# Kernel optimization log

Measured on AMD Instinct MI355X. Metric: run time of the kernel, lower is better.

Reference implementation:

```python
import jax, jax.numpy as jnp
import numpy as np

N = 100000   # nodes
E = 1600000  # edges
D = 128      # d_model
H = 8        # heads
HD = D // H  # head dim
T = 8        # edge types


def setup_inputs() -> dict:
    key = jax.random.key(0)
    ks = jax.random.split(key, 16)
    s = 0.02
    inp = {
        "x": jax.random.normal(ks[0], (N, D), jnp.float32),
        "edge_index": jax.random.randint(ks[1], (2, E), 0, N, jnp.int32),
        "edge_type": jax.random.randint(ks[2], (E,), 0, T, jnp.int32),
        "Wq": jax.random.normal(ks[3], (D, D), jnp.float32) * s,
        "bq": jnp.zeros((D,), jnp.float32),
        "Wk": jax.random.normal(ks[4], (D, D), jnp.float32) * s,
        "bk": jnp.zeros((D,), jnp.float32),
        "Wv": jax.random.normal(ks[5], (D, D), jnp.float32) * s,
        "bv": jnp.zeros((D,), jnp.float32),
        "Wo": jax.random.normal(ks[6], (D, D), jnp.float32) * s,
        "bo": jnp.zeros((D,), jnp.float32),
        "edge_bias": jax.random.normal(ks[7], (T, H), jnp.float32) * s,
        "W1": jax.random.normal(ks[8], (D, D), jnp.float32) * s,
        "b1": jnp.zeros((D,), jnp.float32),
        "W2": jax.random.normal(ks[9], (D, D), jnp.float32) * s,
        "b2": jnp.zeros((D,), jnp.float32),
        "g1": jnp.ones((D,), jnp.float32),
        "be1": jnp.zeros((D,), jnp.float32),
        "g2": jnp.ones((D,), jnp.float32),
        "be2": jnp.zeros((D,), jnp.float32),
    }
    return inp


def _layernorm(x, g, b, eps=1e-5):
    m = jnp.mean(x, axis=-1, keepdims=True)
    v = jnp.mean((x - m) ** 2, axis=-1, keepdims=True)
    return (x - m) * jax.lax.rsqrt(v + eps) * g + b


def reference(x, edge_index, edge_type, Wq, bq, Wk, bk, Wv, bv, Wo, bo,
              edge_bias, W1, b1, W2, b2, g1, be1, g2, be2):
    n = x.shape[0]
    scale = HD ** -0.5
    Q = (x @ Wq + bq).reshape(n, H, HD)
    K = (x @ Wk + bk).reshape(n, H, HD)
    V = (x @ Wv + bv).reshape(n, H, HD)
    src, dst = edge_index[0], edge_index[1]
    # per-edge attention logits [E, H]
    attn = jnp.sum(Q[dst] * K[src], axis=-1) * scale + edge_bias[edge_type]
    # segment softmax grouped by destination node
    mx = jax.ops.segment_max(attn, dst, num_segments=n)  # [n, H]
    ex = jnp.exp(attn - mx[dst])
    sm = jax.ops.segment_sum(ex, dst, num_segments=n)
    a = ex / (sm[dst] + 1e-16)
    # weighted scatter-add of values
    out = jax.ops.segment_sum(a[..., None] * V[src], dst, num_segments=n)
    out = out.reshape(n, D) @ Wo + bo
    x = _layernorm(x + out, g1, be1)
    ffn = jax.nn.gelu(x @ W1 + b1, approximate=False) @ W2 + b2
    return _layernorm(x + ffn, g2, be2)
```

## Files before the change

### kernel.cpp

```cpp
#include <hip/hip_runtime.h>
#include <math.h>

#define D   128
#define NH  8
#define CAP 64

typedef __attribute__((ext_vector_type(8))) short  bfrag;
typedef __attribute__((ext_vector_type(4))) float  f32x4;

__device__ __forceinline__ unsigned short f2bf(float f) {
  unsigned int u = __float_as_uint(f);
  unsigned int r = u + 0x7fffu + ((u >> 16) & 1u);
  return (unsigned short)(r >> 16);
}
__device__ __forceinline__ float bf2f(unsigned short b) {
  return __uint_as_float(((unsigned int)b) << 16);
}

__device__ __forceinline__ int swz(int r, int kb) {
  return r * 256 + (kb ^ ((r & 7) << 4));
}

__global__ void prew_kernel(const float* __restrict__ W0, const float* __restrict__ W1,
                            const float* __restrict__ W2, const float* __restrict__ W3,
                            const float* __restrict__ W4, const float* __restrict__ W5,
                            unsigned short* __restrict__ img)
{
  const float* Wm[6] = {W0, W1, W2, W3, W4, W5};
  const float* W = Wm[blockIdx.x];
  unsigned short* ih = img + (size_t)blockIdx.x * 32768;
  unsigned short* il = ih + 16384;
  for (int s = threadIdx.x; s < 16384; s += 256) {
    int j = s & 7, l = (s >> 3) & 63, kk = (s >> 9) & 3, cbg = s >> 11;
    int c = cbg * 16 + (l & 15);
    int k = kk * 32 + (l >> 4) * 8 + j;
    float v = W[k * D + c];
    unsigned short h = f2bf(v);
    ih[s] = h;
    il[s] = f2bf(v - bf2f(h));
  }
}

__device__ __forceinline__ void stage_x(const float* __restrict__ A, char* lds,
                                        int r0, int n, int t)
{
#pragma unroll
  for (int i = 0; i < 8; ++i) {
    int f = i * 256 + t;
    int r = f >> 5;
    int c = (f & 31) * 4;
    float4 v = make_float4(0.f, 0.f, 0.f, 0.f);
    int row = r0 + r;
    if (row < n) v = *(const float4*)&A[(size_t)row * D + c];
    unsigned short h0 = f2bf(v.x), h1 = f2bf(v.y), h2 = f2bf(v.z), h3 = f2bf(v.w);
    ushort4 hv; hv.x = h0; hv.y = h1; hv.z = h2; hv.w = h3;
    ushort4 lv;
    lv.x = f2bf(v.x - bf2f(h0)); lv.y = f2bf(v.y - bf2f(h1));
    lv.z = f2bf(v.z - bf2f(h2)); lv.w = f2bf(v.w - bf2f(h3));
    int o = swz(r, c * 2);
    *(ushort4*)(lds + o)         = hv;
    *(ushort4*)(lds + 16384 + o) = lv;
  }
}

__device__ __forceinline__ void gemm_tile(const unsigned short* __restrict__ imgh,
                                          const unsigned short* __restrict__ imgl,
                                          const char* lds, f32x4 (&acc)[4][2],
                                          int wave, int lane)
{
  bfrag bh[2][4], bl[2][4];
#pragma unroll
  for (int cb = 0; cb < 2; ++cb)
#pragma unroll
    for (int kk = 0; kk < 4; ++kk) {
      int f = ((wave * 2 + cb) * 4 + kk) * 64 + lane;
      bh[cb][kk] = *(const bfrag*)&imgh[f * 8];
      bl[cb][kk] = *(const bfrag*)&imgl[f * 8];
    }
#pragma unroll
  for (int rb = 0; rb < 4; ++rb)
#pragma unroll
    for (int kk = 0; kk < 4; ++kk) {
      int o = swz(rb * 16 + (lane & 15), kk * 64 + (lane >> 4) * 16);
      bfrag ah = *(const bfrag*)(lds + o);
      bfrag al = *(const bfrag*)(lds + 16384 + o);
#pragma unroll
      for (int cb = 0; cb < 2; ++cb) {
        acc[rb][cb] = __builtin_amdgcn_mfma_f32_16x16x32_bf16(ah, bh[cb][kk], acc[rb][cb], 0, 0, 0);
        acc[rb][cb] = __builtin_amdgcn_mfma_f32_16x16x32_bf16(al, bh[cb][kk], acc[rb][cb], 0, 0, 0);
        acc[rb][cb] = __builtin_amdgcn_mfma_f32_16x16x32_bf16(ah, bl[cb][kk], acc[rb][cb], 0, 0, 0);
      }
    }
}

__device__ __forceinline__ void zero_acc(f32x4 (&acc)[4][2]) {
#pragma unroll
  for (int rb = 0; rb < 4; ++rb)
#pragma unroll
    for (int cb = 0; cb < 2; ++cb) {
      f32x4 z = {0.f, 0.f, 0.f, 0.f};
      acc[rb][cb] = z;
    }
}

__global__ __launch_bounds__(256, 2) void qkv_kernel(
    const float* __restrict__ x, const unsigned short* __restrict__ img,
    const float* __restrict__ bq, const float* __restrict__ bk, const float* __restrict__ bv,
    unsigned short* __restrict__ Q, unsigned short* __restrict__ K,
    unsigned short* __restrict__ V, int n)
{
  __shared__ char lds[49152];
  const int t = threadIdx.x, wave = t >> 6, lane = t & 63;
  const int r0 = blockIdx.x * 64;
  stage_x(x, lds, r0, n, t);
  __syncthreads();

  const float* bs[3] = {bq, bk, bv};
  unsigned short* Os[3] = {Q, K, V};
  unsigned short* scH = (unsigned short*)(lds + 32768);

  for (int m = 0; m < 3; ++m) {
    f32x4 acc[4][2];
    zero_acc(acc);
    gemm_tile(img + (size_t)m * 32768, img + (size_t)m * 32768 + 16384, lds, acc, wave, lane);
    float b0 = bs[m][wave * 32 + (lane & 15)];
    float b1 = bs[m][wave * 32 + 16 + (lane & 15)];
    __syncthreads();
#pragma unroll
    for (int rb = 0; rb < 4; ++rb)
#pragma unroll
      for (int cb = 0; cb < 2; ++cb) {
        float bb = cb ? b1 : b0;
        int col = wave * 32 + cb * 16 + (lane & 15);
#pragma unroll
        for (int r = 0; r < 4; ++r) {
          int row = rb * 16 + (lane >> 4) * 4 + r;
          scH[row * D + col] = f2bf(acc[rb][cb][r] + bb);
        }
      }
    __syncthreads();
#pragma unroll
    for (int i = 0; i < 8; ++i) {
      int f = i * 256 + t;
      int row = f >> 5, c4 = (f & 31) * 4;
      if (r0 + row < n)
        *(ushort4*)&Os[m][(size_t)(r0 + row) * D + c4] = *(ushort4*)&scH[row * D + c4];
    }
  }
}

__global__ __launch_bounds__(256, 2) void gemm_ln_kernel(
    const float* __restrict__ A, const unsigned short* __restrict__ imgh,
    const unsigned short* __restrict__ imgl, const float* __restrict__ bias,
    const float* __restrict__ res, const float* __restrict__ g,
    const float* __restrict__ be, float* out, int n)
{
  __shared__ char lds[32768];
  const int t = threadIdx.x, wave = t >> 6, lane = t & 63;
  const int r0 = blockIdx.x * 64;
  stage_x(A, lds, r0, n, t);
  __syncthreads();
  f32x4 acc[4][2];
  zero_acc(acc);
  gemm_tile(imgh, imgl, lds, acc, wave, lane);
  float b0 = bias[wave * 32 + (lane & 15)];
  float b1 = bias[wave * 32 + 16 + (lane & 15)];
  __syncthreads();
  float* scF = (float*)lds;
#pragma unroll
  for (int rb = 0; rb < 4; ++rb)
#pragma unroll
    for (int cb = 0; cb < 2; ++cb) {
      float bb = cb ? b1 : b0;
      int col = wave * 32 + cb * 16 + (lane & 15);
#pragma unroll
      for (int r = 0; r < 4; ++r) {
        int row = rb * 16 + (lane >> 4) * 4 + r;
        scF[row * D + col] = acc[rb][cb][r] + bb;
      }
    }
  __syncthreads();
  const int tc = t & 31, tr = t >> 5;
  float4 g4  = *(const float4*)&g[tc * 4];
  float4 be4 = *(const float4*)&be[tc * 4];
#pragma unroll
  for (int i = 0; i < 8; ++i) {
    int row = tr * 8 + i;
    int grow = r0 + row;
    float4 y = *(float4*)&scF[row * D + tc * 4];
    float4 rv = make_float4(0.f, 0.f, 0.f, 0.f);
    if (grow < n) rv = *(const float4*)&res[(size_t)grow * D + tc * 4];
    float y0 = y.x + rv.x, y1 = y.y + rv.y, y2 = y.z + rv.z, y3 = y.w + rv.w;
    float sum = y0 + y1 + y2 + y3;
#pragma unroll
    for (int off = 16; off; off >>= 1) sum += __shfl_xor(sum, off);
    float mean = sum * (1.f / 128.f);
    float d0 = y0 - mean, d1 = y1 - mean, d2 = y2 - mean, d3 = y3 - mean;
    float sq = d0 * d0 + d1 * d1 + d2 * d2 + d3 * d3;
#pragma unroll
    for (int off = 16; off; off >>= 1) sq += __shfl_xor(sq, off);
    float inv = 1.0f / sqrtf(sq * (1.f / 128.f) + 1e-5f);
    if (grow < n) {
      float4 o;
      o.x = d0 * inv * g4.x + be4.x; o.y = d1 * inv * g4.y + be4.y;
      o.z = d2 * inv * g4.z + be4.z; o.w = d3 * inv * g4.w + be4.w;
      *(float4*)&out[(size_t)grow * D + tc * 4] = o;
    }
  }
}

__global__ __launch_bounds__(256, 2) void gemm_gelu_kernel(
    const float* __restrict__ A, const unsigned short* __restrict__ imgh,
    const unsigned short* __restrict__ imgl, const float* __restrict__ bias,
    float* __restrict__ out, int n)
{
  __shared__ char lds[32768];
  const int t = threadIdx.x, wave = t >> 6, lane = t & 63;
  const int r0 = blockIdx.x * 64;
  stage_x(A, lds, r0, n, t);
  __syncthreads();
  f32x4 acc[4][2];
  zero_acc(acc);
  gemm_tile(imgh, imgl, lds, acc, wave, lane);
  float b0 = bias[wave * 32 + (lane & 15)];
  float b1 = bias[wave * 32 + 16 + (lane & 15)];
  __syncthreads();
  float* scF = (float*)lds;
#pragma unroll
  for (int rb = 0; rb < 4; ++rb)
#pragma unroll
    for (int cb = 0; cb < 2; ++cb) {
      float bb = cb ? b1 : b0;
      int col = wave * 32 + cb * 16 + (lane & 15);
#pragma unroll
      for (int r = 0; r < 4; ++r) {
        int row = rb * 16 + (lane >> 4) * 4 + r;
        scF[row * D + col] = acc[rb][cb][r] + bb;
      }
    }
  __syncthreads();
#pragma unroll
  for (int i = 0; i < 8; ++i) {
    int f = i * 256 + t;
    int row = f >> 5, c4 = (f & 31) * 4;
    int grow = r0 + row;
    if (grow < n) {
      float4 y = *(float4*)&scF[row * D + c4];
      const float kc = 0.70710678118654752f;
      float4 o;
      o.x = 0.5f * y.x * (1.f + erff(y.x * kc));
      o.y = 0.5f * y.y * (1.f + erff(y.y * kc));
      o.z = 0.5f * y.z * (1.f + erff(y.z * kc));
      o.w = 0.5f * y.w * (1.f + erff(y.w * kc));
      *(float4*)&out[(size_t)grow * D + c4] = o;
    }
  }
}

__global__ void fill_kernel(const int* __restrict__ ei, int* __restrict__ cnt,
                            int* __restrict__ eids, int n, int e)
{
  int i = blockIdx.x * blockDim.x + threadIdx.x;
  if (i < e) {
    int d   = ei[e + i];
    int pos = atomicAdd(&cnt[d], 1);
    if (pos < CAP) eids[(size_t)d * CAP + pos] = i;
  }
}

__global__ __launch_bounds__(256) void attn_kernel(
    const unsigned short* __restrict__ Q, const unsigned short* __restrict__ K,
    const unsigned short* __restrict__ V, const int* __restrict__ ei,
    const int* __restrict__ et, const float* __restrict__ ebias,
    const int* __restrict__ cnt, const int* __restrict__ eids,
    float* __restrict__ out, int n)
{
  const int wave = threadIdx.x >> 6, lane = threadIdx.x & 63;
  const int node = blockIdx.x * 4 + wave;
  if (node >= n) return;
  const int l5 = lane & 31, half = lane >> 5;
  const int d0 = l5 * 4;
  const int h  = l5 >> 2;

  int deg = cnt[node];
  if (deg > CAP) deg = CAP;

  unsigned int packed = 0u;
  if (lane < deg) {
    int eid = eids[(size_t)node * CAP + lane];
    packed = (unsigned)ei[eid] | ((unsigned)et[eid] << 24);
  }

  ushort4 qv = *(const ushort4*)&Q[(size_t)node * D + d0];
  const float scale = 0.25f;
  float q0 = bf2f(qv.x) * scale, q1 = bf2f(qv.y) * scale;
  float q2 = bf2f(qv.z) * scale, q3 = bf2f(qv.w) * scale;

  float s = 0.f, a0 = 0.f, a1 = 0.f, a2 = 0.f, a3 = 0.f;

  unsigned pk = __shfl(packed, half);
  for (int j = 0; j < deg; j += 2) {
    int jj = j + half;
    unsigned cur = pk;
    int nidx = jj + 2; if (nidx > 63) nidx = 63;
    pk = __shfl(packed, nidx);
    int src = (int)(cur & 0xFFFFFFu);
    int ty  = (int)(cur >> 24);
    ushort4 kv = *(const ushort4*)&K[(size_t)src * D + d0];
    ushort4 vv = *(const ushort4*)&V[(size_t)src * D + d0];
    float dot = q0 * bf2f(kv.x) + q1 * bf2f(kv.y) + q2 * bf2f(kv.z) + q3 * bf2f(kv.w);
    dot += __shfl_xor(dot, 1);
    dot += __shfl_xor(dot, 2);
    float logit = dot + ebias[ty * NH + h];
    float p = (jj < deg) ? __expf(logit) : 0.f;
    s  += p;
    a0 += p * bf2f(vv.x); a1 += p * bf2f(vv.y);
    a2 += p * bf2f(vv.z); a3 += p * bf2f(vv.w);
  }
  s  += __shfl_xor(s, 32);
  a0 += __shfl_xor(a0, 32); a1 += __shfl_xor(a1, 32);
  a2 += __shfl_xor(a2, 32); a3 += __shfl_xor(a3, 32);
  if (half == 0) {
    float inv = 1.f / (s + 1e-16f);
    float4 o = make_float4(a0 * inv, a1 * inv, a2 * inv, a3 * inv);
    *(float4*)&out[(size_t)node * D + d0] = o;
  }
}

extern "C" void kernel_launch(void* const* d_in, const int* in_sizes, int n_in,
                              void* d_out, int out_size, void* d_ws, size_t ws_size,
                              hipStream_t stream)
{
  const float* x   = (const float*)d_in[0];
  const int*   ei  = (const int*)  d_in[1];
  const int*   et  = (const int*)  d_in[2];
  const float* Wq  = (const float*)d_in[3];
  const float* bq  = (const float*)d_in[4];
  const float* Wk  = (const float*)d_in[5];
  const float* bk  = (const float*)d_in[6];
  const float* Wv  = (const float*)d_in[7];
  const float* bv  = (const float*)d_in[8];
  const float* Wo  = (const float*)d_in[9];
  const float* bo  = (const float*)d_in[10];
  const float* eb  = (const float*)d_in[11];
  const float* W1  = (const float*)d_in[12];
  const float* b1  = (const float*)d_in[13];
  const float* W2  = (const float*)d_in[14];
  const float* b2  = (const float*)d_in[15];
  const float* g1  = (const float*)d_in[16];
  const float* be1 = (const float*)d_in[17];
  const float* g2  = (const float*)d_in[18];
  const float* be2 = (const float*)d_in[19];

  const int n = in_sizes[0] / D;
  const int e = in_sizes[2];
  const size_t nd = (size_t)n * D;

  unsigned short* Qb = (unsigned short*)d_ws;
  unsigned short* Kb = Qb + nd;
  unsigned short* Vb = Kb + nd;
  float* AO   = (float*)(Vb + nd);
  int*   eids = (int*)(AO + nd);
  int*   cnt  = eids + (size_t)n * CAP;
  unsigned short* img = (unsigned short*)(cnt + n);
  float* hb = (float*)Qb;

  hipMemsetAsync(cnt, 0, (size_t)n * sizeof(int), stream);

  const int gb = (n + 63) / 64;
  prew_kernel<<<6, 256, 0, stream>>>(Wq, Wk, Wv, Wo, W1, W2, img);
  fill_kernel<<<(e + 255) / 256, 256, 0, stream>>>(ei, cnt, eids, n, e);
  qkv_kernel<<<gb, 256, 0, stream>>>(x, img, bq, bk, bv, Qb, Kb, Vb, n);
  attn_kernel<<<(n + 3) / 4, 256, 0, stream>>>(Qb, Kb, Vb, ei, et, eb, cnt, eids, AO, n);
  gemm_ln_kernel<<<gb, 256, 0, stream>>>(AO, img + 3 * 32768, img + 3 * 32768 + 16384,
                                         bo, x, g1, be1, AO, n);
  gemm_gelu_kernel<<<gb, 256, 0, stream>>>(AO, img + 4 * 32768, img + 4 * 32768 + 16384,
                                           b1, hb, n);
  gemm_ln_kernel<<<gb, 256, 0, stream>>>(hb, img + 5 * 32768, img + 5 * 32768 + 16384,
                                         b2, AO, g2, be2, (float*)d_out, n);
}
```

Before: 568.1 us.

## Fuse output projection, FFN and layernorms into one kernel; pack edges at fill time

The three post-attention GEMM kernels (Wo+LN1, W1+GELU, W2+LN2) are merged into one ffn_kernel. Intermediates stay in LDS as bf16 hi/lo split tiles, and the LN1 output is kept in registers for the second residual, which removes several full N×D fp32 global round-trips. The fill kernel now writes packed src|type words directly, so attention no longer does an indirect gather through edge ids. Attention switches to 16 lanes per edge with 8-wide bf16 loads, 4 edges in flight and edge bias cached in LDS. The cost is more LDS per block (about 66KB) and higher register pressure, which may reduce occupancy.

```diff
diff --git a/kernel.cpp b/kernel.cpp
--- a/kernel.cpp
+++ b/kernel.cpp
@@ -4,9 +4,11 @@
 #define D   128
 #define NH  8
 #define CAP 64
+#define SCW 132
 
 typedef __attribute__((ext_vector_type(8))) short  bfrag;
 typedef __attribute__((ext_vector_type(4))) float  f32x4;
+typedef __attribute__((ext_vector_type(8))) unsigned short u16x8;
 
 __device__ __forceinline__ unsigned short f2bf(float f) {
   unsigned int u = __float_as_uint(f);
@@ -103,6 +105,39 @@
     }
 }
 
+__device__ __forceinline__ void store_scF(const f32x4 (&acc)[4][2], float* scF,
+                                          const float* __restrict__ bias,
+                                          int wave, int lane)
+{
+  float b0 = bias[wave * 32 + (lane & 15)];
+  float b1 = bias[wave * 32 + 16 + (lane & 15)];
+#pragma unroll
+  for (int rb = 0; rb < 4; ++rb)
+#pragma unroll
+    for (int cb = 0; cb < 2; ++cb) {
+      float bb = cb ? b1 : b0;
+      int col = wave * 32 + cb * 16 + (lane & 15);
+#pragma unroll
+      for (int r = 0; r < 4; ++r) {
+        int row = rb * 16 + (lane >> 4) * 4 + r;
+        scF[row * SCW + col] = acc[rb][cb][r] + bb;
+      }
+    }
+}
+
+__device__ __forceinline__ void write_bufA4(char* lds, int row, int tc,
+                                            float v0, float v1, float v2, float v3)
+{
+  unsigned short h0 = f2bf(v0), h1 = f2bf(v1), h2 = f2bf(v2), h3 = f2bf(v3);
+  ushort4 hv; hv.x = h0; hv.y = h1; hv.z = h2; hv.w = h3;
+  ushort4 lv;
+  lv.x = f2bf(v0 - bf2f(h0)); lv.y = f2bf(v1 - bf2f(h1));
+  lv.z = f2bf(v2 - bf2f(h2)); lv.w = f2bf(v3 - bf2f(h3));
+  int o = swz(row, tc * 8);
+  *(ushort4*)(lds + o)         = hv;
+  *(ushort4*)(lds + 16384 + o) = lv;
+}
+
 __global__ __launch_bounds__(256, 2) void qkv_kernel(
     const float* __restrict__ x, const unsigned short* __restrict__ img,
     const float* __restrict__ bq, const float* __restrict__ bk, const float* __restrict__ bv,
@@ -149,181 +184,182 @@
   }
 }
 
-__global__ __launch_bounds__(256, 2) void gemm_ln_kernel(
-    const float* __restrict__ A, const unsigned short* __restrict__ imgh,
-    const unsigned short* __restrict__ imgl, const float* __restrict__ bias,
-    const float* __restrict__ res, const float* __restrict__ g,
-    const float* __restrict__ be, float* out, int n)
-{
-  __shared__ char lds[32768];
+__global__ __launch_bounds__(256, 2) void ffn_kernel(
+    const float* __restrict__ AO, const unsigned short* __restrict__ img,
+    const float* __restrict__ x,
+    const float* __restrict__ bo, const float* __restrict__ b1, const float* __restrict__ b2,
+    const float* __restrict__ g1, const float* __restrict__ be1,
+    const float* __restrict__ g2, const float* __restrict__ be2,
+    float* __restrict__ out, int n)
+{
+  __shared__ char lds[32768 + 64 * SCW * 4];
+  float* scF = (float*)(lds + 32768);
   const int t = threadIdx.x, wave = t >> 6, lane = t & 63;
   const int r0 = blockIdx.x * 64;
-  stage_x(A, lds, r0, n, t);
-  __syncthreads();
+  const int tc = t & 31, tr = t >> 5;
+
+  stage_x(AO, lds, r0, n, t);
+  __syncthreads();
+
   f32x4 acc[4][2];
+
   zero_acc(acc);
-  gemm_tile(imgh, imgl, lds, acc, wave, lane);
-  float b0 = bias[wave * 32 + (lane & 15)];
-  float b1 = bias[wave * 32 + 16 + (lane & 15)];
-  __syncthreads();
-  float* scF = (float*)lds;
-#pragma unroll
-  for (int rb = 0; rb < 4; ++rb)
-#pragma unroll
-    for (int cb = 0; cb < 2; ++cb) {
-      float bb = cb ? b1 : b0;
-      int col = wave * 32 + cb * 16 + (lane & 15);
-#pragma unroll
-      for (int r = 0; r < 4; ++r) {
-        int row = rb * 16 + (lane >> 4) * 4 + r;
-        scF[row * D + col] = acc[rb][cb][r] + bb;
-      }
-    }
-  __syncthreads();
-  const int tc = t & 31, tr = t >> 5;
-  float4 g4  = *(const float4*)&g[tc * 4];
-  float4 be4 = *(const float4*)&be[tc * 4];
+  gemm_tile(img + 3 * 32768, img + 3 * 32768 + 16384, lds, acc, wave, lane);
+  store_scF(acc, scF, bo, wave, lane);
+  __syncthreads();
+
+  float x1v[8][4];
+  {
+    float4 g4  = *(const float4*)&g1[tc * 4];
+    float4 be4 = *(const float4*)&be1[tc * 4];
+#pragma unroll
+    for (int i = 0; i < 8; ++i) {
+      int row = tr * 8 + i, grow = r0 + row;
+      float4 y = *(float4*)&scF[row * SCW + tc * 4];
+      float4 rv = make_float4(0.f, 0.f, 0.f, 0.f);
+      if (grow < n) rv = *(const float4*)&x[(size_t)grow * D + tc * 4];
+      float y0 = y.x + rv.x, y1 = y.y + rv.y, y2 = y.z + rv.z, y3 = y.w + rv.w;
+      float sum = y0 + y1 + y2 + y3;
+#pragma unroll
+      for (int off = 16; off; off >>= 1) sum += __shfl_xor(sum, off);
+      float mean = sum * (1.f / 128.f);
+      float d0 = y0 - mean, d1 = y1 - mean, d2 = y2 - mean, d3 = y3 - mean;
+      float sq = d0 * d0 + d1 * d1 + d2 * d2 + d3 * d3;
+#pragma unroll
+      for (int off = 16; off; off >>= 1) sq += __shfl_xor(sq, off);
+      float inv = 1.0f / sqrtf(sq * (1.f / 128.f) + 1e-5f);
+      float v0 = d0 * inv * g4.x + be4.x, v1 = d1 * inv * g4.y + be4.y;
+      float v2 = d2 * inv * g4.z + be4.z, v3 = d3 * inv * g4.w + be4.w;
+      x1v[i][0] = v0; x1v[i][1] = v1; x1v[i][2] = v2; x1v[i][3] = v3;
+      write_bufA4(lds, row, tc, v0, v1, v2, v3);
+    }
+  }
+  __syncthreads();
+
+  zero_acc(acc);
+  gemm_tile(img + 4 * 32768, img + 4 * 32768 + 16384, lds, acc, wave, lane);
+  store_scF(acc, scF, b1, wave, lane);
+  __syncthreads();
 #pragma unroll
   for (int i = 0; i < 8; ++i) {
     int row = tr * 8 + i;
-    int grow = r0 + row;
-    float4 y = *(float4*)&scF[row * D + tc * 4];
-    float4 rv = make_float4(0.f, 0.f, 0.f, 0.f);
-    if (grow < n) rv = *(const float4*)&res[(size_t)grow * D + tc * 4];
-    float y0 = y.x + rv.x, y1 = y.y + rv.y, y2 = y.z + rv.z, y3 = y.w + rv.w;
-    float sum = y0 + y1 + y2 + y3;
-#pragma unroll
-    for (int off = 16; off; off >>= 1) sum += __shfl_xor(sum, off);
-    float mean = sum * (1.f / 128.f);
-    float d0 = y0 - mean, d1 = y1 - mean, d2 = y2 - mean, d3 = y3 - mean;
-    float sq = d0 * d0 + d1 * d1 + d2 * d2 + d3 * d3;
-#pragma unroll
-    for (int off = 16; off; off >>= 1) sq += __shfl_xor(sq, off);
-    float inv = 1.0f / sqrtf(sq * (1.f / 128.f) + 1e-5f);
-    if (grow < n) {
-      float4 o;
-      o.x = d0 * inv * g4.x + be4.x; o.y = d1 * inv * g4.y + be4.y;
-      o.z = d2 * inv * g4.z + be4.z; o.w = d3 * inv * g4.w + be4.w;
-      *(float4*)&out[(size_t)grow * D + tc * 4] = o;
-    }
-  }
-}
-
-__global__ __launch_bounds__(256, 2) void gemm_gelu_kernel(
-    const float* __restrict__ A, const unsigned short* __restrict__ imgh,
-    const unsigned short* __restrict__ imgl, const float* __restrict__ bias,
-    float* __restrict__ out, int n)
-{
-  __shared__ char lds[32768];
-  const int t = threadIdx.x, wave = t >> 6, lane = t & 63;
-  const int r0 = blockIdx.x * 64;
-  stage_x(A, lds, r0, n, t);
-  __syncthreads();
-  f32x4 acc[4][2];
+    float4 y = *(float4*)&scF[row * SCW + tc * 4];
+    const float kc = 0.70710678118654752f;
+    float v0 = 0.5f * y.x * (1.f + erff(y.x * kc));
+    float v1 = 0.5f * y.y * (1.f + erff(y.y * kc));
+    float v2 = 0.5f * y.z * (1.f + erff(y.z * kc));
+    float v3 = 0.5f * y.w * (1.f + erff(y.w * kc));
+    write_bufA4(lds, row, tc, v0, v1, v2, v3);
+  }
+  __syncthreads();
+
   zero_acc(acc);
-  gemm_tile(imgh, imgl, lds, acc, wave, lane);
-  float b0 = bias[wave * 32 + (lane & 15)];
-  float b1 = bias[wave * 32 + 16 + (lane & 15)];
-  __syncthreads();
-  float* scF = (float*)lds;
-#pragma unroll
-  for (int rb = 0; rb < 4; ++rb)
-#pragma unroll
-    for (int cb = 0; cb < 2; ++cb) {
-      float bb = cb ? b1 : b0;
-      int col = wave * 32 + cb * 16 + (lane & 15);
-#pragma unroll
-      for (int r = 0; r < 4; ++r) {
-        int row = rb * 16 + (lane >> 4) * 4 + r;
-        scF[row * D + col] = acc[rb][cb][r] + bb;
+  gemm_tile(img + 5 * 32768, img + 5 * 32768 + 16384, lds, acc, wave, lane);
+  store_scF(acc, scF, b2, wave, lane);
+  __syncthreads();
+  {
+    float4 g4  = *(const float4*)&g2[tc * 4];
+    float4 be4 = *(const float4*)&be2[tc * 4];
+#pragma unroll
+    for (int i = 0; i < 8; ++i) {
+      int row = tr * 8 + i, grow = r0 + row;
+      float4 y = *(float4*)&scF[row * SCW + tc * 4];
+      float y0 = y.x + x1v[i][0], y1 = y.y + x1v[i][1];
+      float y2 = y.z + x1v[i][2], y3 = y.w + x1v[i][3];
+      float sum = y0 + y1 + y2 + y3;
+#pragma unroll
+      for (int off = 16; off; off >>= 1) sum += __shfl_xor(sum, off);
+      float mean = sum * (1.f / 128.f);
+      float d0 = y0 - mean, d1 = y1 - mean, d2 = y2 - mean, d3 = y3 - mean;
+      float sq = d0 * d0 + d1 * d1 + d2 * d2 + d3 * d3;
+#pragma unroll
+      for (int off = 16; off; off >>= 1) sq += __shfl_xor(sq, off);
+      float inv = 1.0f / sqrtf(sq * (1.f / 128.f) + 1e-5f);
+      if (grow < n) {
+        float4 o;
+        o.x = d0 * inv * g4.x + be4.x; o.y = d1 * inv * g4.y + be4.y;
+        o.z = d2 * inv * g4.z + be4.z; o.w = d3 * inv * g4.w + be4.w;
+        *(float4*)&out[(size_t)grow * D + tc * 4] = o;
       }
     }
-  __syncthreads();
-#pragma unroll
-  for (int i = 0; i < 8; ++i) {
-    int f = i * 256 + t;
-    int row = f >> 5, c4 = (f & 31) * 4;
-    int grow = r0 + row;
-    if (grow < n) {
-      float4 y = *(float4*)&scF[row * D + c4];
-      const float kc = 0.70710678118654752f;
-      float4 o;
-      o.x = 0.5f * y.x * (1.f + erff(y.x * kc));
-      o.y = 0.5f * y.y * (1.f + erff(y.y * kc));
-      o.z = 0.5f * y.z * (1.f + erff(y.z * kc));
-      o.w = 0.5f * y.w * (1.f + erff(y.w * kc));
-      *(float4*)&out[(size_t)grow * D + c4] = o;
-    }
-  }
-}
-
-__global__ void fill_kernel(const int* __restrict__ ei, int* __restrict__ cnt,
-                            int* __restrict__ eids, int n, int e)
+  }
+}
+
+__global__ void fill_kernel(const int* __restrict__ ei, const int* __restrict__ et,
+                            int* __restrict__ cnt, unsigned* __restrict__ bucket,
+                            int n, int e)
 {
   int i = blockIdx.x * blockDim.x + threadIdx.x;
   if (i < e) {
-    int d   = ei[e + i];
+    int s  = ei[i];
+    int d  = ei[e + i];
+    int ty = et[i];
     int pos = atomicAdd(&cnt[d], 1);
-    if (pos < CAP) eids[(size_t)d * CAP + pos] = i;
+    if (pos < CAP) bucket[(size_t)d * CAP + pos] = (unsigned)s | ((unsigned)ty << 24);
   }
 }
 
 __global__ __launch_bounds__(256) void attn_kernel(
     const unsigned short* __restrict__ Q, const unsigned short* __restrict__ K,
-    const unsigned short* __restrict__ V, const int* __restrict__ ei,
-    const int* __restrict__ et, const float* __restrict__ ebias,
-    const int* __restrict__ cnt, const int* __restrict__ eids,
+    const unsigned short* __restrict__ V, const float* __restrict__ ebias,
+    const int* __restrict__ cnt, const unsigned* __restrict__ bucket,
     float* __restrict__ out, int n)
 {
+  __shared__ float eb_s[64];
+  if (threadIdx.x < 64) eb_s[threadIdx.x] = ebias[threadIdx.x];
+  __syncthreads();
+
   const int wave = threadIdx.x >> 6, lane = threadIdx.x & 63;
   const int node = blockIdx.x * 4 + wave;
   if (node >= n) return;
-  const int l5 = lane & 31, half = lane >> 5;
-  const int d0 = l5 * 4;
-  const int h  = l5 >> 2;
+
+  const int g  = lane >> 4;
+  const int l  = lane & 15;
+  const int d0 = l * 8;
+  const int h  = l >> 1;
 
   int deg = cnt[node];
   if (deg > CAP) deg = CAP;
 
-  unsigned int packed = 0u;
-  if (lane < deg) {
-    int eid = eids[(size_t)node * CAP + lane];
-    packed = (unsigned)ei[eid] | ((unsigned)et[eid] << 24);
-  }
-
-  ushort4 qv = *(const ushort4*)&Q[(size_t)node * D + d0];
-  const float scale = 0.25f;
-  float q0 = bf2f(qv.x) * scale, q1 = bf2f(qv.y) * scale;
-  float q2 = bf2f(qv.z) * scale, q3 = bf2f(qv.w) * scale;
-
-  float s = 0.f, a0 = 0.f, a1 = 0.f, a2 = 0.f, a3 = 0.f;
-
-  unsigned pk = __shfl(packed, half);
-  for (int j = 0; j < deg; j += 2) {
-    int jj = j + half;
-    unsigned cur = pk;
-    int nidx = jj + 2; if (nidx > 63) nidx = 63;
-    pk = __shfl(packed, nidx);
+  unsigned packed = 0u;
+  if (lane < deg) packed = bucket[(size_t)node * CAP + lane];
+
+  u16x8 qv = *(const u16x8*)&Q[(size_t)node * D + d0];
+  float q[8];
+#pragma unroll
+  for (int i = 0; i < 8; ++i) q[i] = bf2f(qv[i]) * 0.25f;
+
+  float s = 0.f, a[8];
+#pragma unroll
+  for (int i = 0; i < 8; ++i) a[i] = 0.f;
+
+  for (int j = 0; j < deg; j += 4) {
+    int slot = j + g;
+    unsigned cur = __shfl(packed, slot < 63 ? slot : 63);
     int src = (int)(cur & 0xFFFFFFu);
     int ty  = (int)(cur >> 24);
-    ushort4 kv = *(const ushort4*)&K[(size_t)src * D + d0];
-    ushort4 vv = *(const ushort4*)&V[(size_t)src * D + d0];
-    float dot = q0 * bf2f(kv.x) + q1 * bf2f(kv.y) + q2 * bf2f(kv.z) + q3 * bf2f(kv.w);
+    u16x8 kv = *(const u16x8*)&K[(size_t)src * D + d0];
+    u16x8 vv = *(const u16x8*)&V[(size_t)src * D + d0];
+    float dot = 0.f;
+#pragma unroll
+    for (int i = 0; i < 8; ++i) dot += q[i] * bf2f(kv[i]);
     dot += __shfl_xor(dot, 1);
-    dot += __shfl_xor(dot, 2);
-    float logit = dot + ebias[ty * NH + h];
-    float p = (jj < deg) ? __expf(logit) : 0.f;
-    s  += p;
-    a0 += p * bf2f(vv.x); a1 += p * bf2f(vv.y);
-    a2 += p * bf2f(vv.z); a3 += p * bf2f(vv.w);
-  }
-  s  += __shfl_xor(s, 32);
-  a0 += __shfl_xor(a0, 32); a1 += __shfl_xor(a1, 32);
-  a2 += __shfl_xor(a2, 32); a3 += __shfl_xor(a3, 32);
-  if (half == 0) {
+    float logit = dot + eb_s[ty * NH + h];
+    float p = (slot < deg) ? __expf(logit) : 0.f;
+    s += p;
+#pragma unroll
+    for (int i = 0; i < 8; ++i) a[i] += p * bf2f(vv[i]);
+  }
+  s += __shfl_xor(s, 16); s += __shfl_xor(s, 32);
+#pragma unroll
+  for (int i = 0; i < 8; ++i) { a[i] += __shfl_xor(a[i], 16); a[i] += __shfl_xor(a[i], 32); }
+
+  if (g == 0) {
     float inv = 1.f / (s + 1e-16f);
-    float4 o = make_float4(a0 * inv, a1 * inv, a2 * inv, a3 * inv);
-    *(float4*)&out[(size_t)node * D + d0] = o;
+    float4 o0 = make_float4(a[0] * inv, a[1] * inv, a[2] * inv, a[3] * inv);
+    float4 o1 = make_float4(a[4] * inv, a[5] * inv, a[6] * inv, a[7] * inv);
+    *(float4*)&out[(size_t)node * D + d0]     = o0;
+    *(float4*)&out[(size_t)node * D + d0 + 4] = o1;
   }
 }
 
@@ -359,23 +395,18 @@
   unsigned short* Qb = (unsigned short*)d_ws;
   unsigned short* Kb = Qb + nd;
   unsigned short* Vb = Kb + nd;
-  float* AO   = (float*)(Vb + nd);
-  int*   eids = (int*)(AO + nd);
-  int*   cnt  = eids + (size_t)n * CAP;
+  float*    AO     = (float*)(Vb + nd);
+  unsigned* bucket = (unsigned*)(AO + nd);
+  int*      cnt    = (int*)(bucket + (size_t)n * CAP);
   unsigned short* img = (unsigned short*)(cnt + n);
-  float* hb = (float*)Qb;
 
   hipMemsetAsync(cnt, 0, (size_t)n * sizeof(int), stream);
 
   const int gb = (n + 63) / 64;
   prew_kernel<<<6, 256, 0, stream>>>(Wq, Wk, Wv, Wo, W1, W2, img);
-  fill_kernel<<<(e + 255) / 256, 256, 0, stream>>>(ei, cnt, eids, n, e);
+  fill_kernel<<<(e + 255) / 256, 256, 0, stream>>>(ei, et, cnt, bucket, n, e);
   qkv_kernel<<<gb, 256, 0, stream>>>(x, img, bq, bk, bv, Qb, Kb, Vb, n);
-  attn_kernel<<<(n + 3) / 4, 256, 0, stream>>>(Qb, Kb, Vb, ei, et, eb, cnt, eids, AO, n);
-  gemm_ln_kernel<<<gb, 256, 0, stream>>>(AO, img + 3 * 32768, img + 3 * 32768 + 16384,
-                                         bo, x, g1, be1, AO, n);
-  gemm_gelu_kernel<<<gb, 256, 0, stream>>>(AO, img + 4 * 32768, img + 4 * 32768 + 16384,
-                                           b1, hb, n);
-  gemm_ln_kernel<<<gb, 256, 0, stream>>>(hb, img + 5 * 32768, img + 5 * 32768 + 16384,
-                                         b2, AO, g2, be2, (float*)d_out, n);
-}
+  attn_kernel<<<(n + 3) / 4, 256, 0, stream>>>(Qb, Kb, Vb, eb, cnt, bucket, AO, n);
+  ffn_kernel<<<gb, 256, 0, stream>>>(AO, img, x, bo, b1, b2, g1, be1, g2, be2,
+                                     (float*)d_out, n);
+}
```

Result: faster. 512.4 us (-9.8%).
